# Kernel optimization log

Measured on AMD Instinct MI355X. Metric: run time of the kernel, lower is better.

The kernel has to match this reference:

```python
import jax, jax.numpy as jnp
import numpy as np
from jax import lax

B, H, W = 8, 2048, 2048

def _conv3x3(x, w):
    # x: [B,H,W,1], w: [3,3,1,1] (HWIO), SAME padding, stride 1
    return lax.conv_general_dilated(
        x, w, window_strides=(1, 1), padding='SAME',
        dimension_numbers=('NHWC', 'HWIO', 'NHWC'))

def setup_inputs() -> dict:
    key = jax.random.key(0)
    k1, k2, k3, k4, k5, k6 = jax.random.split(key, 6)
    x = jax.random.normal(k1, (B, H, W, 1), dtype=jnp.float32)
    mask = jax.random.randint(k2, (B, H, W, 1), 0, 2, dtype=jnp.int32)
    w1 = jax.random.normal(k3, (3, 3, 1, 1), dtype=jnp.float32)
    b1 = jax.random.normal(k4, (1,), dtype=jnp.float32)
    w2 = jax.random.normal(k5, (3, 3, 1, 1), dtype=jnp.float32)
    b2 = jax.random.normal(k6, (1,), dtype=jnp.float32)
    return {"x": x, "mask": mask, "w1": w1, "b1": b1, "w2": w2, "b2": b2}

def reference(x, mask, w1, b1, w2, b2):
    # Stride-1 MinkowskiConvolution on a sparse 2D tensor == dense 3x3 conv over
    # features zeroed at unoccupied coords, with bias + output restricted to the
    # occupied coordinate set (out_coords == in_coords for stride 1).
    m = mask.astype(x.dtype)                       # occupancy [B,H,W,1]
    h = (_conv3x3(x * m, w1) + b1) * m             # conv1 + bias on active coords
    h = jax.nn.relu(h)                             # MinkowskiReLU (per active coord)
    out = (_conv3x3(h, w2) + b2) * m               # conv2 + bias on active coords
    return out
```

## Files before the change

### kernel.cpp

```cpp
#include <hip/hip_runtime.h>


#define TB_W 128
#define TB_H 16
#define SX   136
#define SY   20
#define NV4  (SX / 4)
#define NSTG (SY * NV4)
#define HR   18
#define NQR  33
#define NQ   (HR * NQR)
#define IMG_W 2048
#define IMG_H 2048

typedef float vf4 __attribute__((ext_vector_type(4)));

__device__ __forceinline__ unsigned pack_bf16_rtn(float a, float b) {
    unsigned ua = __float_as_uint(a), ub = __float_as_uint(b);
    ua = (ua + 0x8000u) >> 16;
    ub = (ub + 0x8000u) & 0xFFFF0000u;
    return ua | ub;
}
__device__ __forceinline__ float bf_lo(unsigned u) { return __uint_as_float(u << 16); }
__device__ __forceinline__ float bf_hi(unsigned u) { return __uint_as_float(u & 0xFFFF0000u); }

__global__ __launch_bounds__(256) void fused_mconv2(
    const float* __restrict__ x, const int* __restrict__ mask,
    const float* __restrict__ w1p, const float* __restrict__ b1p,
    const float* __restrict__ w2p, const float* __restrict__ b2p,
    float* __restrict__ out)
{
    __shared__ __align__(16) unsigned s_xm[SY][SX / 2];
    __shared__ __align__(16) float    s_hm[HR][SX];
    __shared__ __align__(4)  unsigned char s_mb[HR][SX];

    const int hw   = (blockIdx.z * gridDim.y + blockIdx.y) * gridDim.x + blockIdx.x;
    const int xcd  = hw & 7;
    const int slot = hw >> 3;
    const int orig = (xcd << 11) + slot;
    const int ty   = orig & 127;
    const int cl   = orig >> 7;
    const int tx   = cl & 15;
    const int tz   = cl >> 4;

    const int tid  = threadIdx.y * 64 + threadIdx.x;
    const int c0   = tx * TB_W;
    const int row0 = ty * TB_H;
    const size_t plane = (size_t)IMG_W * IMG_H;
    const float* xb = x    + (size_t)tz * plane;
    const int*   mb = mask + (size_t)tz * plane;
    float*       ob = out  + (size_t)tz * plane;

    float W1[9], W2[9];
    #pragma unroll
    for (int i = 0; i < 9; ++i) { W1[i] = w1p[i]; W2[i] = w2p[i]; }
    const float B1 = b1p[0], B2 = b2p[0];

    for (int idx = tid; idx < NSTG; idx += 256) {
        const int row  = idx / NV4;
        const int col4 = idx - row * NV4;
        const int r = row0 - 2 + row;
        const int c = c0 - 4 + (col4 << 2);
        float4 xm = make_float4(0.f, 0.f, 0.f, 0.f);
        unsigned mpack = 0u;
        if (r >= 0 && r < IMG_H && c >= 0 && c < IMG_W) {
            const size_t g = (size_t)r * IMG_W + c;
            const float4 xv = *reinterpret_cast<const float4*>(xb + g);
            const int4   mi = *reinterpret_cast<const int4*>(mb + g);
            xm.x = mi.x ? xv.x : 0.f;
            xm.y = mi.y ? xv.y : 0.f;
            xm.z = mi.z ? xv.z : 0.f;
            xm.w = mi.w ? xv.w : 0.f;
            mpack = (mi.x ? 1u : 0u) | (mi.y ? 256u : 0u) |
                    (mi.z ? 65536u : 0u) | (mi.w ? 16777216u : 0u);
        }
        uint2 p;
        p.x = pack_bf16_rtn(xm.x, xm.y);
        p.y = pack_bf16_rtn(xm.z, xm.w);
        *reinterpret_cast<uint2*>(&s_xm[row][col4 << 1]) = p;
        if (row >= 1 && row <= HR)
            *reinterpret_cast<unsigned*>(&s_mb[row - 1][col4 << 2]) = mpack;
    }
    __syncthreads();

    for (int idx = tid; idx < NQ; idx += 256) {
        const int hr = idx / NQR;
        const int q  = idx - hr * NQR;
        const int hc = q << 2;
        float a0 = B1, a1 = B1, a2 = B1, a3 = B1;
        #pragma unroll
        for (int di = 0; di < 3; ++di) {
            const unsigned* xr = &s_xm[hr + di][q << 1];
            const uint2 A  = *reinterpret_cast<const uint2*>(xr);
            const uint2 Bv = *reinterpret_cast<const uint2*>(xr + 2);
            const float c2 = bf_lo(A.y),  c3 = bf_hi(A.y);
            const float c4 = bf_lo(Bv.x), c5 = bf_hi(Bv.x);
            const float c6 = bf_lo(Bv.y), c7 = bf_hi(Bv.y);
            const float w0 = W1[di * 3], w1 = W1[di * 3 + 1], w2 = W1[di * 3 + 2];
            a0 += w0 * c2 + w1 * c3 + w2 * c4;
            a1 += w0 * c3 + w1 * c4 + w2 * c5;
            a2 += w0 * c4 + w1 * c5 + w2 * c6;
            a3 += w0 * c5 + w1 * c6 + w2 * c7;
        }
        const unsigned mA = *reinterpret_cast<const unsigned*>(&s_mb[hr][hc]);
        const unsigned mB = *reinterpret_cast<const unsigned*>(&s_mb[hr][hc + 4]);
        float4 e;
        e.x = ((mA >> 24) & 255u) ? fmaxf(a0, 0.f) : -1.0f;
        e.y = ( mB        & 255u) ? fmaxf(a1, 0.f) : -1.0f;
        e.z = ((mB >>  8) & 255u) ? fmaxf(a2, 0.f) : -1.0f;
        e.w = ((mB >> 16) & 255u) ? fmaxf(a3, 0.f) : -1.0f;
        *reinterpret_cast<float4*>(&s_hm[hr][hc]) = e;
    }
    __syncthreads();

    {
        const int q     = tid & 31;
        const int strip = tid >> 5;
        const int i0    = strip << 1;
        const int jc    = q << 2;
        float P[4] = {0,0,0,0}, Q[4] = {0,0,0,0}, cm[4] = {0,0,0,0};
        #pragma unroll
        for (int t = 0; t < 4; ++t) {
            const int hr = i0 + t;
            const float4 E1 = *reinterpret_cast<const float4*>(&s_hm[hr][jc]);
            const float4 E2 = *reinterpret_cast<const float4*>(&s_hm[hr][jc + 4]);
            const float v0 = E1.x, v1 = E1.y, v2 = E1.z, v3 = E1.w;
            const float v4 = E2.x, v5 = E2.y;
            const float r0 = fmaxf(v0, 0.f), r1 = fmaxf(v1, 0.f);
            const float r2 = fmaxf(v2, 0.f), r3 = fmaxf(v3, 0.f);
            const float r4 = fmaxf(v4, 0.f), r5 = fmaxf(v5, 0.f);
            float d0[4], d1[4], d2[4];
            d0[0] = W2[0]*r0 + W2[1]*r1 + W2[2]*r2;
            d0[1] = W2[0]*r1 + W2[1]*r2 + W2[2]*r3;
            d0[2] = W2[0]*r2 + W2[1]*r3 + W2[2]*r4;
            d0[3] = W2[0]*r3 + W2[1]*r4 + W2[2]*r5;
            d1[0] = W2[3]*r0 + W2[4]*r1 + W2[5]*r2;
            d1[1] = W2[3]*r1 + W2[4]*r2 + W2[5]*r3;
            d1[2] = W2[3]*r2 + W2[4]*r3 + W2[5]*r4;
            d1[3] = W2[3]*r3 + W2[4]*r4 + W2[5]*r5;
            d2[0] = W2[6]*r0 + W2[7]*r1 + W2[8]*r2;
            d2[1] = W2[6]*r1 + W2[7]*r2 + W2[8]*r3;
            d2[2] = W2[6]*r2 + W2[7]*r3 + W2[8]*r4;
            d2[3] = W2[6]*r3 + W2[7]*r4 + W2[8]*r5;
            if (t >= 2) {
                const int i = i0 + t - 2;
                vf4 o;
                o.x = (cm[0] >= 0.f) ? (Q[0] + d2[0] + B2) : 0.f;
                o.y = (cm[1] >= 0.f) ? (Q[1] + d2[1] + B2) : 0.f;
                o.z = (cm[2] >= 0.f) ? (Q[2] + d2[2] + B2) : 0.f;
                o.w = (cm[3] >= 0.f) ? (Q[3] + d2[3] + B2) : 0.f;
                __builtin_nontemporal_store(
                    o, reinterpret_cast<vf4*>(
                           ob + (size_t)(row0 + i) * IMG_W + (c0 + jc)));
            }
            #pragma unroll
            for (int c = 0; c < 4; ++c) { Q[c] = P[c] + d1[c]; P[c] = d0[c]; }
            cm[0] = v1; cm[1] = v2; cm[2] = v3; cm[3] = v4;
        }
    }
}

extern "C" void kernel_launch(void* const* d_in, const int* in_sizes, int n_in,
                              void* d_out, int out_size, void* d_ws, size_t ws_size,
                              hipStream_t stream) {
    const float* x    = (const float*)d_in[0];
    const int*   mask = (const int*)  d_in[1];
    const float* w1   = (const float*)d_in[2];
    const float* b1   = (const float*)d_in[3];
    const float* w2   = (const float*)d_in[4];
    const float* b2   = (const float*)d_in[5];
    float*       out  = (float*)d_out;

    dim3 block(64, 4, 1);
    dim3 grid(IMG_W / TB_W, IMG_H / TB_H, 8);
    hipLaunchKernelGGL(fused_mconv2, grid, block, 0, stream,
                       x, mask, w1, b1, w2, b2, out);
}
```

Measured before the change: 71.91 us.

## Process two row tiles per block with register-prefetched global loads

Each block now handles two vertically adjacent 16-row tiles. Global loads for the second tile are issued into registers while conv1 of the first tile runs, and conv2 of the first tile overlaps the shared-memory staging of the second. Loads use clamped addresses, so they need no branches, and the grid becomes a flat 1D launch with a matching XCD swizzle. This aims to hide global memory latency, but it adds register pressure and halves the number of blocks.

New measurement: 75.24 us. 1.05x slower.

```diff
diff --git a/kernel.cpp b/kernel.cpp
--- a/kernel.cpp
+++ b/kernel.cpp
@@ -34,18 +34,19 @@
     __shared__ __align__(16) float    s_hm[HR][SX];
     __shared__ __align__(4)  unsigned char s_mb[HR][SX];
 
-    const int hw   = (blockIdx.z * gridDim.y + blockIdx.y) * gridDim.x + blockIdx.x;
+    const int hw   = blockIdx.x;
     const int xcd  = hw & 7;
     const int slot = hw >> 3;
-    const int orig = (xcd << 11) + slot;
-    const int ty   = orig & 127;
-    const int cl   = orig >> 7;
+    const int orig = (xcd << 10) + slot;
+    const int band = orig & 63;
+    const int cl   = orig >> 6;
     const int tx   = cl & 15;
     const int tz   = cl >> 4;
 
     const int tid  = threadIdx.y * 64 + threadIdx.x;
     const int c0   = tx * TB_W;
-    const int row0 = ty * TB_H;
+    const int r0A  = band * (2 * TB_H);
+    const int r0B  = r0A + TB_H;
     const size_t plane = (size_t)IMG_W * IMG_H;
     const float* xb = x    + (size_t)tz * plane;
     const int*   mb = mask + (size_t)tz * plane;
@@ -56,64 +57,87 @@
     for (int i = 0; i < 9; ++i) { W1[i] = w1p[i]; W2[i] = w2p[i]; }
     const float B1 = b1p[0], B2 = b2p[0];
 
-    for (int idx = tid; idx < NSTG; idx += 256) {
-        const int row  = idx / NV4;
-        const int col4 = idx - row * NV4;
-        const int r = row0 - 2 + row;
-        const int c = c0 - 4 + (col4 << 2);
-        float4 xm = make_float4(0.f, 0.f, 0.f, 0.f);
-        unsigned mpack = 0u;
-        if (r >= 0 && r < IMG_H && c >= 0 && c < IMG_W) {
+    float4 xr[3]; int4 mr[3];
+
+    auto issue_loads = [&](int r0t) {
+        #pragma unroll
+        for (int u = 0; u < 3; ++u) {
+            int idx = tid + (u << 8);
+            idx = idx < NSTG ? idx : NSTG - 1;
+            const int row  = idx / NV4;
+            const int col4 = idx - row * NV4;
+            int r = r0t - 2 + row;
+            int c = c0 - 4 + (col4 << 2);
+            r = r < 0 ? 0 : (r > IMG_H - 1 ? IMG_H - 1 : r);
+            c = c < 0 ? 0 : (c > IMG_W - 4 ? IMG_W - 4 : c);
             const size_t g = (size_t)r * IMG_W + c;
-            const float4 xv = *reinterpret_cast<const float4*>(xb + g);
-            const int4   mi = *reinterpret_cast<const int4*>(mb + g);
-            xm.x = mi.x ? xv.x : 0.f;
-            xm.y = mi.y ? xv.y : 0.f;
-            xm.z = mi.z ? xv.z : 0.f;
-            xm.w = mi.w ? xv.w : 0.f;
-            mpack = (mi.x ? 1u : 0u) | (mi.y ? 256u : 0u) |
-                    (mi.z ? 65536u : 0u) | (mi.w ? 16777216u : 0u);
-        }
-        uint2 p;
-        p.x = pack_bf16_rtn(xm.x, xm.y);
-        p.y = pack_bf16_rtn(xm.z, xm.w);
-        *reinterpret_cast<uint2*>(&s_xm[row][col4 << 1]) = p;
-        if (row >= 1 && row <= HR)
-            *reinterpret_cast<unsigned*>(&s_mb[row - 1][col4 << 2]) = mpack;
-    }
-    __syncthreads();
-
-    for (int idx = tid; idx < NQ; idx += 256) {
-        const int hr = idx / NQR;
-        const int q  = idx - hr * NQR;
-        const int hc = q << 2;
-        float a0 = B1, a1 = B1, a2 = B1, a3 = B1;
+            xr[u] = *reinterpret_cast<const float4*>(xb + g);
+            mr[u] = *reinterpret_cast<const int4*>(mb + g);
+        }
+    };
+    auto stage_write = [&](int r0t) {
         #pragma unroll
-        for (int di = 0; di < 3; ++di) {
-            const unsigned* xr = &s_xm[hr + di][q << 1];
-            const uint2 A  = *reinterpret_cast<const uint2*>(xr);
-            const uint2 Bv = *reinterpret_cast<const uint2*>(xr + 2);
-            const float c2 = bf_lo(A.y),  c3 = bf_hi(A.y);
-            const float c4 = bf_lo(Bv.x), c5 = bf_hi(Bv.x);
-            const float c6 = bf_lo(Bv.y), c7 = bf_hi(Bv.y);
-            const float w0 = W1[di * 3], w1 = W1[di * 3 + 1], w2 = W1[di * 3 + 2];
-            a0 += w0 * c2 + w1 * c3 + w2 * c4;
-            a1 += w0 * c3 + w1 * c4 + w2 * c5;
-            a2 += w0 * c4 + w1 * c5 + w2 * c6;
-            a3 += w0 * c5 + w1 * c6 + w2 * c7;
-        }
-        const unsigned mA = *reinterpret_cast<const unsigned*>(&s_mb[hr][hc]);
-        const unsigned mB = *reinterpret_cast<const unsigned*>(&s_mb[hr][hc + 4]);
-        float4 e;
-        e.x = ((mA >> 24) & 255u) ? fmaxf(a0, 0.f) : -1.0f;
-        e.y = ( mB        & 255u) ? fmaxf(a1, 0.f) : -1.0f;
-        e.z = ((mB >>  8) & 255u) ? fmaxf(a2, 0.f) : -1.0f;
-        e.w = ((mB >> 16) & 255u) ? fmaxf(a3, 0.f) : -1.0f;
-        *reinterpret_cast<float4*>(&s_hm[hr][hc]) = e;
-    }
-    __syncthreads();
-
-    {
+        for (int u = 0; u < 3; ++u) {
+            const int idx = tid + (u << 8);
+            if (idx < NSTG) {
+                const int row  = idx / NV4;
+                const int col4 = idx - row * NV4;
+                const int r = r0t - 2 + row;
+                const int c = c0 - 4 + (col4 << 2);
+                float4 xm = make_float4(0.f, 0.f, 0.f, 0.f);
+                unsigned mpack = 0u;
+                if (r >= 0 && r < IMG_H && c >= 0 && c < IMG_W) {
+                    const float4 xv = xr[u];
+                    const int4   mi = mr[u];
+                    xm.x = mi.x ? xv.x : 0.f;
+                    xm.y = mi.y ? xv.y : 0.f;
+                    xm.z = mi.z ? xv.z : 0.f;
+                    xm.w = mi.w ? xv.w : 0.f;
+                    mpack = (mi.x ? 1u : 0u) | (mi.y ? 256u : 0u) |
+                            (mi.z ? 65536u : 0u) | (mi.w ? 16777216u : 0u);
+                }
+                uint2 p;
+                p.x = pack_bf16_rtn(xm.x, xm.y);
+                p.y = pack_bf16_rtn(xm.z, xm.w);
+                *reinterpret_cast<uint2*>(&s_xm[row][col4 << 1]) = p;
+                if (row >= 1 && row <= HR)
+                    *reinterpret_cast<unsigned*>(&s_mb[row - 1][col4 << 2]) = mpack;
+            }
+        }
+    };
+
+    auto conv1 = [&]() {
+        for (int idx = tid; idx < NQ; idx += 256) {
+            const int hr = idx / NQR;
+            const int q  = idx - hr * NQR;
+            const int hc = q << 2;
+            float a0 = B1, a1 = B1, a2 = B1, a3 = B1;
+            #pragma unroll
+            for (int di = 0; di < 3; ++di) {
+                const unsigned* xrp = &s_xm[hr + di][q << 1];
+                const uint2 A  = *reinterpret_cast<const uint2*>(xrp);
+                const uint2 Bv = *reinterpret_cast<const uint2*>(xrp + 2);
+                const float c2 = bf_lo(A.y),  c3 = bf_hi(A.y);
+                const float c4 = bf_lo(Bv.x), c5 = bf_hi(Bv.x);
+                const float c6 = bf_lo(Bv.y), c7 = bf_hi(Bv.y);
+                const float w0 = W1[di * 3], w1 = W1[di * 3 + 1], w2 = W1[di * 3 + 2];
+                a0 += w0 * c2 + w1 * c3 + w2 * c4;
+                a1 += w0 * c3 + w1 * c4 + w2 * c5;
+                a2 += w0 * c4 + w1 * c5 + w2 * c6;
+                a3 += w0 * c5 + w1 * c6 + w2 * c7;
+            }
+            const unsigned mA = *reinterpret_cast<const unsigned*>(&s_mb[hr][hc]);
+            const unsigned mB = *reinterpret_cast<const unsigned*>(&s_mb[hr][hc + 4]);
+            float4 e;
+            e.x = ((mA >> 24) & 255u) ? fmaxf(a0, 0.f) : -1.0f;
+            e.y = ( mB        & 255u) ? fmaxf(a1, 0.f) : -1.0f;
+            e.z = ((mB >>  8) & 255u) ? fmaxf(a2, 0.f) : -1.0f;
+            e.w = ((mB >> 16) & 255u) ? fmaxf(a3, 0.f) : -1.0f;
+            *reinterpret_cast<float4*>(&s_hm[hr][hc]) = e;
+        }
+    };
+
+    auto conv2 = [&](int r0t) {
         const int q     = tid & 31;
         const int strip = tid >> 5;
         const int i0    = strip << 1;
@@ -151,13 +175,30 @@
                 o.w = (cm[3] >= 0.f) ? (Q[3] + d2[3] + B2) : 0.f;
                 __builtin_nontemporal_store(
                     o, reinterpret_cast<vf4*>(
-                           ob + (size_t)(row0 + i) * IMG_W + (c0 + jc)));
+                           ob + (size_t)(r0t + i) * IMG_W + (c0 + jc)));
             }
             #pragma unroll
             for (int c = 0; c < 4; ++c) { Q[c] = P[c] + d1[c]; P[c] = d0[c]; }
             cm[0] = v1; cm[1] = v2; cm[2] = v3; cm[3] = v4;
         }
-    }
+    };
+
+    issue_loads(r0A);
+    stage_write(r0A);
+    __syncthreads();
+
+    issue_loads(r0B);
+    conv1();
+    __syncthreads();
+
+    stage_write(r0B);
+    conv2(r0A);
+    __syncthreads();
+
+    conv1();
+    __syncthreads();
+
+    conv2(r0B);
 }
 
 extern "C" void kernel_launch(void* const* d_in, const int* in_sizes, int n_in,
@@ -172,7 +213,7 @@
     float*       out  = (float*)d_out;
 
     dim3 block(64, 4, 1);
-    dim3 grid(IMG_W / TB_W, IMG_H / TB_H, 8);
+    dim3 grid(8192, 1, 1);
     hipLaunchKernelGGL(fused_mconv2, grid, block, 0, stream,
                        x, mask, w1, b1, w2, b2, out);
 }
```
